# Kernel optimization log

Hardware: AMD Instinct MI355X
Metric: run time of the kernel (lower is better)

## Reference

```python
import jax, jax.numpy as jnp
import numpy as np

D = 160          # SDF grid resolution (D1=D2=D3=D)
LEVEL = 0.0      # marching_cubes(-sdf, level=-0) == level 0 on s = -sdf
N_SMOOTH = 2
LAMBD = 1.0


def _extract_mesh_np():
    """Host-side isosurface extraction (mirrors the module's CPU round-trip).
    Uses marching tetrahedra (6-tet cube decomposition) in place of skimage's
    lewiner marching cubes; topo_correct (undefined in source) is identity.
    Returns (verts [V,3] f32 in normalized coords, faces [F,3] i32, edges [E,2] i32).
    """
    xs = np.arange(D, dtype=np.float32)
    X, Y, Z = np.meshgrid(xs, xs, xs, indexing='ij')
    ctr = (D - 1) / 2.0
    sdf = np.sqrt((X - ctr) ** 2 + (Y - ctr) ** 2 + (Z - ctr) ** 2) - 0.35 * D
    sdf = sdf + 3.0 * np.sin(0.20 * X) * np.sin(0.17 * Y) * np.sin(0.23 * Z)
    s = (-sdf).astype(np.float32)  # extract level-0 isosurface of -sdf
    sflat = s.ravel()
    Ng = D ** 3

    corner_off = [(0, 0, 0), (1, 0, 0), (1, 1, 0), (0, 1, 0),
                  (0, 0, 1), (1, 0, 1), (1, 1, 1), (0, 1, 1)]
    b = np.arange(D - 1)
    BX, BY, BZ = np.meshgrid(b, b, b, indexing='ij')
    BX, BY, BZ = BX.ravel(), BY.ravel(), BZ.ravel()
    gid8 = [((BX + dx) * D + (BY + dy)) * D + (BZ + dz) for dx, dy, dz in corner_off]
    val8 = [sflat[g] for g in gid8]

    TETS = [(0, 5, 1, 6), (0, 1, 2, 6), (0, 2, 3, 6),
            (0, 3, 7, 6), (0, 7, 4, 6), (0, 4, 5, 6)]
    TE = [(0, 1), (0, 2), (0, 3), (1, 2), (1, 3), (2, 3)]  # tet edges
    CASE_TRIS = {1: [(0, 1, 2)], 14: [(0, 1, 2)],
                 2: [(0, 3, 4)], 13: [(0, 3, 4)],
                 4: [(1, 3, 5)], 11: [(1, 3, 5)],
                 8: [(2, 4, 5)], 7: [(2, 4, 5)],
                 3: [(1, 3, 4), (1, 4, 2)], 12: [(1, 3, 4), (1, 4, 2)],
                 5: [(0, 3, 5), (0, 5, 2)], 10: [(0, 3, 5), (0, 5, 2)],
                 6: [(0, 4, 5), (0, 5, 1)], 9: [(0, 4, 5), (0, 5, 1)]}
    bitw = np.array([1, 2, 4, 8])

    tri_keys = []
    for tet in TETS:
        tv = np.stack([val8[c] for c in tet], 1)  # [Nc,4] corner values
        tg = np.stack([gid8[c] for c in tet], 1)  # [Nc,4] corner grid ids
        case = (tv < LEVEL).astype(np.int64) @ bitw
        for c, tris in CASE_TRIS.items():
            sel = np.nonzero(case == c)[0]
            if sel.size == 0:
                continue
            g = tg[sel]
            for tri in tris:
                cols = []
                for e in tri:
                    i, j = TE[e]
                    lo = np.minimum(g[:, i], g[:, j])
                    hi = np.maximum(g[:, i], g[:, j])
                    cols.append(lo * Ng + hi)  # canonical grid-edge key
                tri_keys.append(np.stack(cols, 1))
    tris = np.concatenate(tri_keys, 0)  # [F,3] edge keys
    uk, inv = np.unique(tris, return_inverse=True)
    faces = inv.reshape(-1, 3).astype(np.int32)
    ga = uk // Ng
    gb = uk % Ng
    pa = np.stack(np.unravel_index(ga, (D, D, D)), 1).astype(np.float32)
    pb = np.stack(np.unravel_index(gb, (D, D, D)), 1).astype(np.float32)
    sa = sflat[ga]
    sb = sflat[gb]
    t = ((LEVEL - sa) / (sb - sa)).astype(np.float32)
    verts = pa + t[:, None] * (pb - pa)
    verts = (2.0 * verts - np.float32(D)) / np.float32(D)  # (2v-[D1,D2,D3])/D
    e = np.concatenate([faces[:, [0, 1]], faces[:, [1, 2]], faces[:, [2, 0]]], 0)
    e = np.unique(np.sort(e, 1), axis=0).astype(np.int32)
    return verts.astype(np.float32), faces, e


def setup_inputs() -> dict:
    verts, faces, edges = _extract_mesh_np()
    return {
        'v': jnp.asarray(verts)[None],      # [1,V,3]
        'edges': jnp.asarray(edges),        # [E,2] unique undirected mesh edges
        'faces': jnp.asarray(faces)[None],  # [1,F,3]
    }


def reference(v, edges, faces):
    # Uniform laplacian smoothing: v <- v + lambd * (mean_neighbor(v) - v), x2
    V = v.shape[1]
    src = jnp.concatenate([edges[:, 0], edges[:, 1]])
    dst = jnp.concatenate([edges[:, 1], edges[:, 0]])
    x = v[0]
    deg = jax.ops.segment_sum(jnp.ones(src.shape[0], x.dtype), src, num_segments=V)
    inv_deg = 1.0 / jnp.maximum(deg, 1.0)
    for _ in range(N_SMOOTH):
        nbr = jax.ops.segment_sum(x[dst], src, num_segments=V)
        x = x + LAMBD * (nbr * inv_deg[:, None] - x)
    return x, faces[0]
```

## Files before the change

### kernel.cpp

```cpp
#include <hip/hip_runtime.h>

#define K_ELL 32
#define K_OVF 16
#define TBS   1024
#define RNG_LOG 11
#define RNG   2048
#define BAND  2048
#define RW    (RNG + BAND)
#define BS    256

__global__ void prep_kernel(const int2* __restrict__ edges, int* __restrict__ offs_a,
                            int* __restrict__ cntN, int* __restrict__ cntF,
                            int* __restrict__ deg_ovf, int E, int V) {
    int i = blockIdx.x * blockDim.x + threadIdx.x;
    if (i <= E) {
        if (i < E) {
            int lo = (i == 0) ? 0 : edges[i - 1].x + 1;
            int hi = edges[i].x;
            for (int a = lo; a <= hi; a++) offs_a[a] = i;
        } else {
            for (int a = edges[E - 1].x + 1; a <= V; a++) offs_a[a] = E;
        }
    }
    if (i < V) deg_ovf[i] = 0;
    if (i <= RNG) cntF[i] = 0;
    if (i == 0) cntN[0] = 0;
}

__global__ __launch_bounds__(TBS) void build_kernel(
        const int2* __restrict__ edges, const int* __restrict__ offs_a,
        int* __restrict__ cntN, int* __restrict__ cntF, int* __restrict__ deg_ovf,
        int* __restrict__ adjN, int* __restrict__ adjF, int* __restrict__ adj_ovf,
        const int* __restrict__ faces, float* __restrict__ out_f,
        const float* __restrict__ v, float4* __restrict__ v4,
        int E, int V, int F3, int NBb) {
    if ((int)blockIdx.x >= NBb) {
        int t = (blockIdx.x - NBb) * TBS + threadIdx.x;
        int T = (gridDim.x - NBb) * TBS;
        for (int j = t; j < F3; j += T) out_f[j] = (float)faces[j];
        for (int u = t; u < V; u += T)
            v4[u] = make_float4(v[3 * u], v[3 * u + 1], v[3 * u + 2], 0.f);
        return;
    }
    __shared__ int cnt[RW];
    const int v0   = blockIdx.x << RNG_LOG;
    const int vEnd = min(v0 + RNG, V);
    for (int i = threadIdx.x; i < RW; i += TBS) cnt[i] = 0;
    const int eBeg = offs_a[v0];
    const int eEnd = offs_a[vEnd];
    __syncthreads();
    for (int i = eBeg + threadIdx.x; i < eEnd; i += TBS) {
        int2 e = edges[i];
        int rel = e.y - (v0 + 1);
        if (rel < RW) {
            int r = atomicAdd(&cnt[rel], 1);
            if (rel < RNG) { if (r < K_ELL) adjN[(size_t)r * V + e.y] = e.x; }
            else           { if (r < K_ELL) adjF[(size_t)r * V + e.y] = e.x; }
        } else {
            int r = atomicAdd(&deg_ovf[e.y], 1);
            if (r < K_OVF) adj_ovf[(size_t)r * V + e.y] = e.x;
        }
    }
    __syncthreads();
    for (int i = threadIdx.x; i < RW; i += TBS) {
        int u = v0 + 1 + i;
        if (u < V) {
            if (i < RNG) cntN[u] = cnt[i];
            else         cntF[u] = cnt[i];
        }
    }
}

template <bool PAD>
__global__ void gather_kernel(const float4* __restrict__ x4, const int2* __restrict__ edges,
                              const int* __restrict__ offs_a,
                              const int* __restrict__ cntN, const int* __restrict__ cntF,
                              const int* __restrict__ deg_ovf,
                              const int* __restrict__ adjN, const int* __restrict__ adjF,
                              const int* __restrict__ adj_ovf,
                              float* __restrict__ y, int V) {
    int u = blockIdx.x * blockDim.x + threadIdx.x;
    if (u >= V) return;
    int aBeg = offs_a[u], aEnd = offs_a[u + 1];
    int cN = cntN[u], cF = cntF[u], dO = deg_ovf[u];
    float s0 = 0.f, s1 = 0.f, s2 = 0.f;
    for (int i = aBeg; i < aEnd; i++) {
        float4 p = x4[edges[i].y];
        s0 += p.x; s1 += p.y; s2 += p.z;
    }
    int kN = cN > K_ELL ? K_ELL : cN;
    for (int k = 0; k < kN; k++) {
        float4 p = x4[adjN[(size_t)k * V + u]];
        s0 += p.x; s1 += p.y; s2 += p.z;
    }
    int kF = cF > K_ELL ? K_ELL : cF;
    for (int k = 0; k < kF; k++) {
        float4 p = x4[adjF[(size_t)k * V + u]];
        s0 += p.x; s1 += p.y; s2 += p.z;
    }
    int kO = dO > K_OVF ? K_OVF : dO;
    for (int k = 0; k < kO; k++) {
        float4 p = x4[adj_ovf[(size_t)k * V + u]];
        s0 += p.x; s1 += p.y; s2 += p.z;
    }
    int d = (aEnd - aBeg) + cN + cF + dO;
    float inv = 1.0f / fmaxf((float)d, 1.0f);
    if (PAD) {
        ((float4*)y)[u] = make_float4(s0 * inv, s1 * inv, s2 * inv, 0.f);
    } else {
        y[3 * u + 0] = s0 * inv;
        y[3 * u + 1] = s1 * inv;
        y[3 * u + 2] = s2 * inv;
    }
}

extern "C" void kernel_launch(void* const* d_in, const int* in_sizes, int n_in,
                              void* d_out, int out_size, void* d_ws, size_t ws_size,
                              hipStream_t stream) {
    const float* v     = (const float*)d_in[0];
    const int2*  edges = (const int2*)d_in[1];
    const int*   faces = (const int*)d_in[2];

    const int V3 = in_sizes[0];
    const int V  = V3 / 3;
    const int E  = in_sizes[1] / 2;
    const int F3 = in_sizes[2];

    float* out_v = (float*)d_out;
    float* out_f = (float*)d_out + V3;

    float4* v4      = (float4*)d_ws;
    float4* x1      = v4 + V;
    int*    adjN    = (int*)(x1 + V);
    int*    adjF    = adjN + (size_t)K_ELL * V;
    int*    adj_ovf = adjF + (size_t)K_ELL * V;
    int*    offs_a  = adj_ovf + (size_t)K_OVF * V;
    int*    cntN    = offs_a + (V + 1);
    int*    cntF    = cntN + (V + 1);
    int*    deg_ovf = cntF + (V + 1);

    const int NBb = (V + RNG - 1) / RNG;
    const int copyElems = F3 > V ? F3 : V;
    const int NBc = (copyElems + TBS - 1) / TBS;
    const int gP  = (E + 1 + BS - 1) / BS;
    const int gV  = (V + BS - 1) / BS;

    prep_kernel<<<gP, BS, 0, stream>>>(edges, offs_a, cntN, cntF, deg_ovf, E, V);

    build_kernel<<<NBb + NBc, TBS, 0, stream>>>(edges, offs_a, cntN, cntF, deg_ovf,
                                                adjN, adjF, adj_ovf, faces, out_f,
                                                v, v4, E, V, F3, NBb);

    gather_kernel<true ><<<gV, BS, 0, stream>>>(v4, edges, offs_a, cntN, cntF, deg_ovf,
                                                adjN, adjF, adj_ovf, (float*)x1, V);
    gather_kernel<false><<<gV, BS, 0, stream>>>(x1, edges, offs_a, cntN, cntF, deg_ovf,
                                                adjN, adjF, adj_ovf, out_v, V);
}
```

Measured before the change: 95.15 us.

## Fuse prep, build and both gathers into one cooperative persistent kernel

Replaces the four launches with one cooperative kernel that uses grid-wide syncs between phases: prep, adjacency build plus face copy, first gather, second gather. The three adjacency arrays are merged into one plane array. Each thread caches its neighbor indices in registers during the first gather and reuses them in the second. This removes launch gaps and repeated index loads, at the cost of grid.sync overhead and a grid capped at 256 blocks of 1024 threads, so each thread loops over several vertices.

```diff
diff --git a/kernel.cpp b/kernel.cpp
--- a/kernel.cpp
+++ b/kernel.cpp
@@ -1,4 +1,8 @@
 #include <hip/hip_runtime.h>
+#include <hip/hip_cooperative_groups.h>
+#include <stdint.h>
+
+namespace cg = cooperative_groups;
 
 #define K_ELL 32
 #define K_OVF 16
@@ -7,110 +11,201 @@
 #define RNG   2048
 #define BAND  2048
 #define RW    (RNG + BAND)
-#define BS    256
-
-__global__ void prep_kernel(const int2* __restrict__ edges, int* __restrict__ offs_a,
-                            int* __restrict__ cntN, int* __restrict__ cntF,
-                            int* __restrict__ deg_ovf, int E, int V) {
-    int i = blockIdx.x * blockDim.x + threadIdx.x;
-    if (i <= E) {
+#define MAXA  8
+#define MAXB  8
+
+__device__ __forceinline__ int planeOf(int k, int kN, int kF) {
+    return (k < kN) ? k
+         : ((k < kN + kF) ? (K_ELL + (k - kN)) : (2 * K_ELL + (k - kN - kF)));
+}
+
+__device__ __forceinline__ float4 gather_one(const float4* __restrict__ x, int u,
+        const int2* __restrict__ edges, const int* __restrict__ offs_a,
+        const int* __restrict__ cntN, const int* __restrict__ cntF,
+        const int* __restrict__ deg_ovf, const int* __restrict__ adjN, int V) {
+    int aBeg = offs_a[u], aEnd = offs_a[u + 1];
+    int cN = cntN[u], cF = cntF[u], dO = deg_ovf[u];
+    int kN = min(cN, K_ELL), kF = min(cF, K_ELL), kO = min(dO, K_OVF);
+    int kB = kN + kF + kO;
+    float s0 = 0.f, s1 = 0.f, s2 = 0.f;
+    for (int i = aBeg; i < aEnd; ++i) {
+        float4 p = x[edges[i].y]; s0 += p.x; s1 += p.y; s2 += p.z;
+    }
+    for (int k = 0; k < kB; ++k) {
+        float4 p = x[adjN[(size_t)planeOf(k, kN, kF) * V + u]];
+        s0 += p.x; s1 += p.y; s2 += p.z;
+    }
+    int d = (aEnd - aBeg) + cN + cF + dO;
+    float inv = 1.0f / fmaxf((float)d, 1.0f);
+    return make_float4(s0 * inv, s1 * inv, s2 * inv, 0.f);
+}
+
+__global__ __launch_bounds__(TBS) void mega_kernel(
+        const int2* __restrict__ edges, int* __restrict__ offs_a,
+        int* __restrict__ cntN, int* __restrict__ cntF, int* __restrict__ deg_ovf,
+        int* __restrict__ adjN,
+        const int* __restrict__ faces, float* __restrict__ out_f,
+        const float* __restrict__ v, float4* __restrict__ v4,
+        float4* __restrict__ x1, float* __restrict__ out_v,
+        int E, int V, int F3, int NBb) {
+    cg::grid_group grid = cg::this_grid();
+    const int NB = (int)gridDim.x;
+    const int NT = NB * TBS;
+    const int t  = (int)blockIdx.x * TBS + (int)threadIdx.x;
+    __shared__ int cnt[RW];
+
+    for (int i = t; i <= E; i += NT) {
         if (i < E) {
             int lo = (i == 0) ? 0 : edges[i - 1].x + 1;
             int hi = edges[i].x;
-            for (int a = lo; a <= hi; a++) offs_a[a] = i;
+            for (int a = lo; a <= hi; ++a) offs_a[a] = i;
         } else {
-            for (int a = edges[E - 1].x + 1; a <= V; a++) offs_a[a] = E;
-        }
-    }
-    if (i < V) deg_ovf[i] = 0;
-    if (i <= RNG) cntF[i] = 0;
-    if (i == 0) cntN[0] = 0;
-}
-
-__global__ __launch_bounds__(TBS) void build_kernel(
-        const int2* __restrict__ edges, const int* __restrict__ offs_a,
-        int* __restrict__ cntN, int* __restrict__ cntF, int* __restrict__ deg_ovf,
-        int* __restrict__ adjN, int* __restrict__ adjF, int* __restrict__ adj_ovf,
-        const int* __restrict__ faces, float* __restrict__ out_f,
-        const float* __restrict__ v, float4* __restrict__ v4,
-        int E, int V, int F3, int NBb) {
-    if ((int)blockIdx.x >= NBb) {
-        int t = (blockIdx.x - NBb) * TBS + threadIdx.x;
-        int T = (gridDim.x - NBb) * TBS;
-        for (int j = t; j < F3; j += T) out_f[j] = (float)faces[j];
-        for (int u = t; u < V; u += T)
+            int lo = (E > 0) ? edges[E - 1].x + 1 : 0;
+            for (int a = lo; a <= V; ++a) offs_a[a] = E;
+        }
+    }
+    for (int i = t; i < V; i += NT) deg_ovf[i] = 0;
+    {
+        int zEnd = RNG < V ? RNG : V;
+        for (int i = t; i <= zEnd; i += NT) cntF[i] = 0;
+    }
+    if (t == 0) cntN[0] = 0;
+    if (((uintptr_t)v & 15) == 0) {
+        const float4* vv = (const float4*)v;
+        int n4 = V >> 2;
+        for (int q = t; q < n4; q += NT) {
+            float4 a = vv[3 * q], b = vv[3 * q + 1], c = vv[3 * q + 2];
+            v4[4 * q + 0] = make_float4(a.x, a.y, a.z, 0.f);
+            v4[4 * q + 1] = make_float4(a.w, b.x, b.y, 0.f);
+            v4[4 * q + 2] = make_float4(b.z, b.w, c.x, 0.f);
+            v4[4 * q + 3] = make_float4(c.y, c.z, c.w, 0.f);
+        }
+        for (int u = (n4 << 2) + t; u < V; u += NT)
             v4[u] = make_float4(v[3 * u], v[3 * u + 1], v[3 * u + 2], 0.f);
-        return;
-    }
-    __shared__ int cnt[RW];
-    const int v0   = blockIdx.x << RNG_LOG;
-    const int vEnd = min(v0 + RNG, V);
-    for (int i = threadIdx.x; i < RW; i += TBS) cnt[i] = 0;
-    const int eBeg = offs_a[v0];
-    const int eEnd = offs_a[vEnd];
-    __syncthreads();
-    for (int i = eBeg + threadIdx.x; i < eEnd; i += TBS) {
-        int2 e = edges[i];
-        int rel = e.y - (v0 + 1);
-        if (rel < RW) {
-            int r = atomicAdd(&cnt[rel], 1);
-            if (rel < RNG) { if (r < K_ELL) adjN[(size_t)r * V + e.y] = e.x; }
-            else           { if (r < K_ELL) adjF[(size_t)r * V + e.y] = e.x; }
-        } else {
-            int r = atomicAdd(&deg_ovf[e.y], 1);
-            if (r < K_OVF) adj_ovf[(size_t)r * V + e.y] = e.x;
-        }
-    }
-    __syncthreads();
-    for (int i = threadIdx.x; i < RW; i += TBS) {
-        int u = v0 + 1 + i;
-        if (u < V) {
-            if (i < RNG) cntN[u] = cnt[i];
-            else         cntF[u] = cnt[i];
-        }
-    }
-}
-
-template <bool PAD>
-__global__ void gather_kernel(const float4* __restrict__ x4, const int2* __restrict__ edges,
-                              const int* __restrict__ offs_a,
-                              const int* __restrict__ cntN, const int* __restrict__ cntF,
-                              const int* __restrict__ deg_ovf,
-                              const int* __restrict__ adjN, const int* __restrict__ adjF,
-                              const int* __restrict__ adj_ovf,
-                              float* __restrict__ y, int V) {
-    int u = blockIdx.x * blockDim.x + threadIdx.x;
-    if (u >= V) return;
-    int aBeg = offs_a[u], aEnd = offs_a[u + 1];
-    int cN = cntN[u], cF = cntF[u], dO = deg_ovf[u];
-    float s0 = 0.f, s1 = 0.f, s2 = 0.f;
-    for (int i = aBeg; i < aEnd; i++) {
-        float4 p = x4[edges[i].y];
-        s0 += p.x; s1 += p.y; s2 += p.z;
-    }
-    int kN = cN > K_ELL ? K_ELL : cN;
-    for (int k = 0; k < kN; k++) {
-        float4 p = x4[adjN[(size_t)k * V + u]];
-        s0 += p.x; s1 += p.y; s2 += p.z;
-    }
-    int kF = cF > K_ELL ? K_ELL : cF;
-    for (int k = 0; k < kF; k++) {
-        float4 p = x4[adjF[(size_t)k * V + u]];
-        s0 += p.x; s1 += p.y; s2 += p.z;
-    }
-    int kO = dO > K_OVF ? K_OVF : dO;
-    for (int k = 0; k < kO; k++) {
-        float4 p = x4[adj_ovf[(size_t)k * V + u]];
-        s0 += p.x; s1 += p.y; s2 += p.z;
-    }
-    int d = (aEnd - aBeg) + cN + cF + dO;
-    float inv = 1.0f / fmaxf((float)d, 1.0f);
-    if (PAD) {
-        ((float4*)y)[u] = make_float4(s0 * inv, s1 * inv, s2 * inv, 0.f);
     } else {
-        y[3 * u + 0] = s0 * inv;
-        y[3 * u + 1] = s1 * inv;
-        y[3 * u + 2] = s2 * inv;
+        for (int u = t; u < V; u += NT)
+            v4[u] = make_float4(v[3 * u], v[3 * u + 1], v[3 * u + 2], 0.f);
+    }
+
+    grid.sync();
+
+    for (int w = (int)blockIdx.x; w < NBb; w += NB) {
+        const int v0   = w << RNG_LOG;
+        const int vEnd = min(v0 + RNG, V);
+        for (int i = threadIdx.x; i < RW; i += TBS) cnt[i] = 0;
+        const int eBeg = offs_a[v0];
+        const int eEnd = offs_a[vEnd];
+        __syncthreads();
+        for (int i = eBeg + (int)threadIdx.x; i < eEnd; i += TBS) {
+            int2 e = edges[i];
+            int rel = e.y - (v0 + 1);
+            if (rel < RW) {
+                int r = atomicAdd(&cnt[rel], 1);
+                if (r < K_ELL)
+                    adjN[(size_t)((rel < RNG) ? r : (K_ELL + r)) * V + e.y] = e.x;
+            } else {
+                int r = atomicAdd(&deg_ovf[e.y], 1);
+                if (r < K_OVF) adjN[(size_t)(2 * K_ELL + r) * V + e.y] = e.x;
+            }
+        }
+        __syncthreads();
+        for (int i = threadIdx.x; i < RW; i += TBS) {
+            int u = v0 + 1 + i;
+            if (u < V) { if (i < RNG) cntN[u] = cnt[i]; else cntF[u] = cnt[i]; }
+        }
+        __syncthreads();
+    }
+    {
+        const int cb0 = (NB > NBb) ? NBb : 0;
+        if ((int)blockIdx.x >= cb0) {
+            int tc = ((int)blockIdx.x - cb0) * TBS + (int)threadIdx.x;
+            int TC = (NB - cb0) * TBS;
+            if ((((uintptr_t)out_f | (uintptr_t)faces) & 15) == 0) {
+                int n4 = F3 >> 2;
+                const int4* f4 = (const int4*)faces;
+                float4* o4 = (float4*)out_f;
+                for (int j = tc; j < n4; j += TC) {
+                    int4 a = f4[j];
+                    o4[j] = make_float4((float)a.x, (float)a.y, (float)a.z, (float)a.w);
+                }
+                for (int j = (n4 << 2) + tc; j < F3; j += TC) out_f[j] = (float)faces[j];
+            } else {
+                for (int j = tc; j < F3; j += TC) out_f[j] = (float)faces[j];
+            }
+        }
+    }
+
+    grid.sync();
+
+    int idxA[MAXA], idxB[MAXB];
+    int da = 0, kN = 0, kF = 0, kB = 0, aBeg = 0;
+    float invd = 0.f;
+    const int u0 = t;
+    if (u0 < V) {
+        aBeg = offs_a[u0];
+        int aEnd = offs_a[u0 + 1];
+        int cN = cntN[u0], cF = cntF[u0], dO = deg_ovf[u0];
+        da = aEnd - aBeg;
+        kN = min(cN, K_ELL); kF = min(cF, K_ELL);
+        int kO = min(dO, K_OVF);
+        kB = kN + kF + kO;
+        int dtrue = da + cN + cF + dO;
+        invd = 1.0f / fmaxf((float)dtrue, 1.0f);
+        float s0 = 0.f, s1 = 0.f, s2 = 0.f;
+        #pragma unroll
+        for (int j = 0; j < MAXA; ++j) {
+            int g = 0;
+            if (j < da) {
+                g = edges[aBeg + j].y;
+                float4 p = v4[g]; s0 += p.x; s1 += p.y; s2 += p.z;
+            }
+            idxA[j] = g;
+        }
+        #pragma unroll
+        for (int k = 0; k < MAXB; ++k) {
+            int g = 0;
+            if (k < kB) {
+                g = adjN[(size_t)planeOf(k, kN, kF) * V + u0];
+                float4 p = v4[g]; s0 += p.x; s1 += p.y; s2 += p.z;
+            }
+            idxB[k] = g;
+        }
+        for (int j = MAXA; j < da; ++j) {
+            float4 p = v4[edges[aBeg + j].y]; s0 += p.x; s1 += p.y; s2 += p.z;
+        }
+        for (int k = MAXB; k < kB; ++k) {
+            float4 p = v4[adjN[(size_t)planeOf(k, kN, kF) * V + u0]];
+            s0 += p.x; s1 += p.y; s2 += p.z;
+        }
+        x1[u0] = make_float4(s0 * invd, s1 * invd, s2 * invd, 0.f);
+    }
+    for (int u = t + NT; u < V; u += NT)
+        x1[u] = gather_one(v4, u, edges, offs_a, cntN, cntF, deg_ovf, adjN, V);
+
+    grid.sync();
+
+    if (u0 < V) {
+        float s0 = 0.f, s1 = 0.f, s2 = 0.f;
+        #pragma unroll
+        for (int j = 0; j < MAXA; ++j)
+            if (j < da) { float4 p = x1[idxA[j]]; s0 += p.x; s1 += p.y; s2 += p.z; }
+        #pragma unroll
+        for (int k = 0; k < MAXB; ++k)
+            if (k < kB) { float4 p = x1[idxB[k]]; s0 += p.x; s1 += p.y; s2 += p.z; }
+        for (int j = MAXA; j < da; ++j) {
+            float4 p = x1[edges[aBeg + j].y]; s0 += p.x; s1 += p.y; s2 += p.z;
+        }
+        for (int k = MAXB; k < kB; ++k) {
+            float4 p = x1[adjN[(size_t)planeOf(k, kN, kF) * V + u0]];
+            s0 += p.x; s1 += p.y; s2 += p.z;
+        }
+        out_v[3 * u0 + 0] = s0 * invd;
+        out_v[3 * u0 + 1] = s1 * invd;
+        out_v[3 * u0 + 2] = s2 * invd;
+    }
+    for (int u = t + NT; u < V; u += NT) {
+        float4 r = gather_one(x1, u, edges, offs_a, cntN, cntF, deg_ovf, adjN, V);
+        out_v[3 * u + 0] = r.x; out_v[3 * u + 1] = r.y; out_v[3 * u + 2] = r.z;
     }
 }
 
@@ -132,27 +227,30 @@
     float4* v4      = (float4*)d_ws;
     float4* x1      = v4 + V;
     int*    adjN    = (int*)(x1 + V);
-    int*    adjF    = adjN + (size_t)K_ELL * V;
-    int*    adj_ovf = adjF + (size_t)K_ELL * V;
-    int*    offs_a  = adj_ovf + (size_t)K_OVF * V;
+    int*    offs_a  = adjN + (size_t)(2 * K_ELL + K_OVF) * V;
     int*    cntN    = offs_a + (V + 1);
     int*    cntF    = cntN + (V + 1);
     int*    deg_ovf = cntF + (V + 1);
 
     const int NBb = (V + RNG - 1) / RNG;
-    const int copyElems = F3 > V ? F3 : V;
-    const int NBc = (copyElems + TBS - 1) / TBS;
-    const int gP  = (E + 1 + BS - 1) / BS;
-    const int gV  = (V + BS - 1) / BS;
-
-    prep_kernel<<<gP, BS, 0, stream>>>(edges, offs_a, cntN, cntF, deg_ovf, E, V);
-
-    build_kernel<<<NBb + NBc, TBS, 0, stream>>>(edges, offs_a, cntN, cntF, deg_ovf,
-                                                adjN, adjF, adj_ovf, faces, out_f,
-                                                v, v4, E, V, F3, NBb);
-
-    gather_kernel<true ><<<gV, BS, 0, stream>>>(v4, edges, offs_a, cntN, cntF, deg_ovf,
-                                                adjN, adjF, adj_ovf, (float*)x1, V);
-    gather_kernel<false><<<gV, BS, 0, stream>>>(x1, edges, offs_a, cntN, cntF, deg_ovf,
-                                                adjN, adjF, adj_ovf, out_v, V);
-}
+
+    static int nbMax = -1;
+    if (nbMax < 0) {
+        int occ = 0, cus = 0, dev = 0;
+        (void)hipGetDevice(&dev);
+        (void)hipOccupancyMaxActiveBlocksPerMultiprocessor(
+                &occ, (const void*)mega_kernel, TBS, 0);
+        (void)hipDeviceGetAttribute(&cus, hipDeviceAttributeMultiprocessorCount, dev);
+        if (occ < 1) occ = 1;
+        if (cus < 1) cus = 256;
+        nbMax = occ * cus;
+    }
+    int NB = nbMax < 256 ? nbMax : 256;
+
+    void* args[] = { (void*)&edges, (void*)&offs_a, (void*)&cntN, (void*)&cntF,
+                     (void*)&deg_ovf, (void*)&adjN, (void*)&faces, (void*)&out_f,
+                     (void*)&v, (void*)&v4, (void*)&x1, (void*)&out_v,
+                     (void*)&E, (void*)&V, (void*)&F3, (void*)&NBb };
+    (void)hipLaunchCooperativeKernel((const void*)mega_kernel, dim3(NB), dim3(TBS),
+                                     args, 0, stream);
+}
```

Result: slower. 189.9 us (+99.6%).
